# Optimization experiments

Measured on AMD Instinct MI355X. Metric: run time of the kernel, lower is better.

## Reference

```python
import jax, jax.numpy as jnp
import numpy as np

N, E, IN_DIM, HID, K, PDIM, NCLS, NHID_LAYERS = 50000, 800000, 128, 64, 3, 2, 16, 3
EPS = 1e-5


def setup_inputs() -> dict:
    key = jax.random.key(0)
    ks = jax.random.split(key, 24)
    d = {
        'feature': jax.random.normal(ks[0], (N, IN_DIM), jnp.float32),
        'emb_w': jax.random.normal(ks[1], (IN_DIM, HID), jnp.float32) * 0.05,
        'emb_b': jnp.zeros((HID,), jnp.float32),
        # 3 identical hidden GMM layers (stacked on leading axis)
        'fc_w': jax.random.normal(ks[2], (NHID_LAYERS, HID, K * HID), jnp.float32) * 0.05,
        'fc_b': jnp.zeros((NHID_LAYERS, K * HID), jnp.float32),
        'mu': jax.random.normal(ks[3], (NHID_LAYERS, K, PDIM), jnp.float32),
        'inv_sigma': jnp.ones((NHID_LAYERS, K, PDIM), jnp.float32) + 0.1 * jax.random.normal(ks[4], (NHID_LAYERS, K, PDIM), jnp.float32),
        'pp_w': jax.random.normal(ks[5], (NHID_LAYERS, 2, PDIM), jnp.float32),
        'pp_b': jnp.zeros((NHID_LAYERS, PDIM), jnp.float32),
        'bn_g': jnp.ones((NHID_LAYERS, HID), jnp.float32),
        'bn_b': jnp.zeros((NHID_LAYERS, HID), jnp.float32),
        # last layer: hidden -> n_classes
        'fc_w_l': jax.random.normal(ks[6], (HID, K * NCLS), jnp.float32) * 0.05,
        'fc_b_l': jnp.zeros((K * NCLS,), jnp.float32),
        'mu_l': jax.random.normal(ks[7], (K, PDIM), jnp.float32),
        'inv_sigma_l': jnp.ones((K, PDIM), jnp.float32) + 0.1 * jax.random.normal(ks[8], (K, PDIM), jnp.float32),
        'pp_w_l': jax.random.normal(ks[9], (2, PDIM), jnp.float32),
        'pp_b_l': jnp.zeros((PDIM,), jnp.float32),
        'bn_g_l': jnp.ones((NCLS,), jnp.float32),
        'bn_b_l': jnp.zeros((NCLS,), jnp.float32),
        'edge_index': jax.random.randint(ks[10], (2, E), 0, N, jnp.int64),
    }
    return d


def _gmm_layer(h, row, col, pseudo, fcw, fcb, mu, isg, bng, bnb, residual):
    n = h.shape[0]
    k, out = mu.shape[0], fcw.shape[1] // mu.shape[0]
    hp = (h @ fcw + fcb).reshape(n, k, out)          # [N,K,out]
    diff = pseudo[:, None, :] - mu                    # [E,K,2]
    gauss = jnp.exp(-0.5 * jnp.sum((diff * isg) ** 2, axis=-1))  # [E,K]
    msg = jnp.einsum('ek,ekc->ec', gauss, hp[row])    # gather src, weight, sum kernels
    agg = jax.ops.segment_sum(msg, col, num_segments=n)  # scatter-add to dst
    mean = jnp.mean(agg, axis=0)
    var = jnp.var(agg, axis=0)
    hbn = (agg - mean) * jax.lax.rsqrt(var + EPS) * bng + bnb  # BN (train stats)
    hnew = jax.nn.relu(hbn)
    if residual:
        hnew = h + hnew
    return hnew  # dropout p=0.0


def reference(feature, emb_w, emb_b, fc_w, fc_b, mu, inv_sigma, pp_w, pp_b, bn_g, bn_b,
              fc_w_l, fc_b_l, mu_l, inv_sigma_l, pp_w_l, pp_b_l, bn_g_l, bn_b_l, edge_index):
    row, col = edge_index[0], edge_index[1]
    n = feature.shape[0]
    ones_e = jnp.ones((row.shape[0],), feature.dtype)
    deg_r = jax.ops.segment_sum(ones_e, row, num_segments=n)
    deg_c = jax.ops.segment_sum(ones_e, col, num_segments=n)
    srcs = jax.lax.rsqrt(deg_r[row] + 1.0)
    dsts = jax.lax.rsqrt(deg_c[col] + 1.0)
    pseudo = jnp.stack([srcs, dsts], axis=-1)  # [E,2]
    h = feature @ emb_w + emb_b
    for i in range(NHID_LAYERS):
        ps = jnp.tanh(pseudo @ pp_w[i] + pp_b[i])
        h = _gmm_layer(h, row, col, ps, fc_w[i], fc_b[i], mu[i], inv_sigma[i], bn_g[i], bn_b[i], residual=True)
    ps = jnp.tanh(pseudo @ pp_w_l + pp_b_l)
    h = _gmm_layer(h, row, col, ps, fc_w_l, fc_b_l, mu_l, inv_sigma_l, bn_g_l, bn_b_l, residual=False)
    return h
```

## Files before the change

kernel.cpp:

```cpp
#include <hip/hip_runtime.h>
#include <cstdint>
#include <cstddef>


#define EPS 1e-5f
#define KAUG 196

__global__ void degree_kernel(const int* __restrict__ rowi, const int* __restrict__ coli,
                              int* __restrict__ dr, int* __restrict__ dc, int E) {
    int i = blockIdx.x * blockDim.x + threadIdx.x;
    int stride = gridDim.x * blockDim.x;
    for (; i < E; i += stride) {
        atomicAdd(&dr[rowi[i]], 1);
        atomicAdd(&dc[coli[i]], 1);
    }
}

__global__ void pseudo_kernel(const int* __restrict__ rowi, const int* __restrict__ coli,
                              const int* __restrict__ dr, const int* __restrict__ dc,
                              float2* __restrict__ pseudo, int E) {
    int i = blockIdx.x * blockDim.x + threadIdx.x;
    int stride = gridDim.x * blockDim.x;
    for (; i < E; i += stride) {
        float a = rsqrtf((float)dr[rowi[i]] + 1.0f);
        float b = rsqrtf((float)dc[coli[i]] + 1.0f);
        pseudo[i] = make_float2(a, b);
    }
}

__global__ __launch_bounds__(256) void scan_phase1(const int* __restrict__ cnt,
                                                   int* __restrict__ partial,
                                                   int* __restrict__ blockSum, int Nn) {
    __shared__ int sm[256];
    int tid = blockIdx.x * 256 + threadIdx.x;
    int v = (tid < Nn) ? cnt[tid] : 0;
    sm[threadIdx.x] = v;
    __syncthreads();
    for (int d = 1; d < 256; d <<= 1) {
        int t = (threadIdx.x >= d) ? sm[threadIdx.x - d] : 0;
        __syncthreads();
        sm[threadIdx.x] += t;
        __syncthreads();
    }
    if (tid < Nn) partial[tid] = sm[threadIdx.x] - v;
    if (threadIdx.x == 255) blockSum[blockIdx.x] = sm[255];
}

__global__ __launch_bounds__(1024) void scan_phase2(const int* __restrict__ blockSum,
                                                    int* __restrict__ blockOff, int B) {
    __shared__ int sm[1024];
    int v = (threadIdx.x < B) ? blockSum[threadIdx.x] : 0;
    sm[threadIdx.x] = v;
    __syncthreads();
    for (int d = 1; d < 1024; d <<= 1) {
        int t = (threadIdx.x >= d) ? sm[threadIdx.x - d] : 0;
        __syncthreads();
        sm[threadIdx.x] += t;
        __syncthreads();
    }
    if (threadIdx.x < B) blockOff[threadIdx.x] = sm[threadIdx.x] - v;
}

__global__ __launch_bounds__(256) void scan_phase3(const int* __restrict__ partial,
                                                   const int* __restrict__ blockOff,
                                                   int* __restrict__ start,
                                                   int* __restrict__ cursor, int Nn) {
    int tid = blockIdx.x * 256 + threadIdx.x;
    if (tid < Nn) {
        int s = partial[tid] + blockOff[blockIdx.x];
        start[tid] = s;
        cursor[tid] = s;
    }
}

__global__ void csr_scatter(const int* __restrict__ rowi, const int* __restrict__ coli,
                            const float2* __restrict__ pseudo, int* __restrict__ cursor,
                            int* __restrict__ rowPerm, float2* __restrict__ pseudoPerm, int E) {
    int i = blockIdx.x * blockDim.x + threadIdx.x;
    int stride = gridDim.x * blockDim.x;
    for (; i < E; i += stride) {
        int d = coli[i];
        int pos = atomicAdd(&cursor[d], 1);
        rowPerm[pos] = rowi[i];
        pseudoPerm[pos] = pseudo[i];
    }
}

__global__ void gauss_kernel(const float2* __restrict__ pseudo,
                             const float* __restrict__ ppw,
                             const float* __restrict__ ppb,
                             const float* __restrict__ mu,
                             const float* __restrict__ isg,
                             float4* __restrict__ gauss, int E) {
    int i = blockIdx.x * blockDim.x + threadIdx.x;
    int stride = gridDim.x * blockDim.x;
    float w00 = ppw[0], w01 = ppw[1], w10 = ppw[2], w11 = ppw[3];
    float b0 = ppb[0], b1 = ppb[1];
    float m00 = mu[0], m01 = mu[1], m10 = mu[2], m11 = mu[3], m20 = mu[4], m21 = mu[5];
    float s00 = isg[0], s01 = isg[1], s10 = isg[2], s11 = isg[3], s20 = isg[4], s21 = isg[5];
    for (; i < E; i += stride) {
        float2 p = pseudo[i];
        float ps0 = tanhf(fmaf(p.y, w10, fmaf(p.x, w00, b0)));
        float ps1 = tanhf(fmaf(p.y, w11, fmaf(p.x, w01, b1)));
        float d0, d1;
        d0 = (ps0 - m00) * s00; d1 = (ps1 - m01) * s01;
        float g0 = expf(-0.5f * (d0 * d0 + d1 * d1));
        d0 = (ps0 - m10) * s10; d1 = (ps1 - m11) * s11;
        float g1 = expf(-0.5f * (d0 * d0 + d1 * d1));
        d0 = (ps0 - m20) * s20; d1 = (ps1 - m21) * s21;
        float g2 = expf(-0.5f * (d0 * d0 + d1 * d1));
        gauss[i] = make_float4(g0, g1, g2, 0.0f);
    }
}

__global__ void w2_transform(const float* __restrict__ fcw, const float* __restrict__ fcb,
                             float* __restrict__ W2, int C) {
    int i = blockIdx.x * blockDim.x + threadIdx.x;
    int tot = KAUG * C;
    if (i >= tot) return;
    int r = i / C, c = i - r * C;
    float v;
    if (r < 192) {
        int k = r >> 6, j = r & 63;
        v = fcw[j * (3 * C) + k * C + c];
    } else if (r < 195) {
        v = fcb[(r - 192) * C + c];
    } else {
        v = 0.0f;
    }
    W2[i] = v;
}

__global__ __launch_bounds__(256) void pull_kernel(const int* __restrict__ start,
                                                   const int* __restrict__ cnt,
                                                   const int* __restrict__ rowPerm,
                                                   const float4* __restrict__ gauss,
                                                   const float* __restrict__ h,
                                                   float* __restrict__ m, int Nn) {
    int wave = threadIdx.x >> 6;
    int lane = threadIdx.x & 63;
    int d = blockIdx.x * 4 + wave;
    if (d >= Nn) return;
    int s = start[d];
    int e = s + cnt[d];
    float a0 = 0.0f, a1 = 0.0f, a2 = 0.0f;
    float s0 = 0.0f, s1 = 0.0f, s2 = 0.0f;
    const float* hl = h + lane;
    int i = s;
    for (; i + 3 < e; i += 4) {
        int r0 = rowPerm[i], r1 = rowPerm[i + 1], r2 = rowPerm[i + 2], r3 = rowPerm[i + 3];
        float4 g0 = gauss[i], g1 = gauss[i + 1], g2 = gauss[i + 2], g3 = gauss[i + 3];
        float h0 = hl[(size_t)r0 * 64], h1 = hl[(size_t)r1 * 64];
        float h2 = hl[(size_t)r2 * 64], h3 = hl[(size_t)r3 * 64];
        a0 = fmaf(g0.x, h0, a0); a1 = fmaf(g0.y, h0, a1); a2 = fmaf(g0.z, h0, a2);
        a0 = fmaf(g1.x, h1, a0); a1 = fmaf(g1.y, h1, a1); a2 = fmaf(g1.z, h1, a2);
        a0 = fmaf(g2.x, h2, a0); a1 = fmaf(g2.y, h2, a1); a2 = fmaf(g2.z, h2, a2);
        a0 = fmaf(g3.x, h3, a0); a1 = fmaf(g3.y, h3, a1); a2 = fmaf(g3.z, h3, a2);
        s0 += g0.x + g1.x + g2.x + g3.x;
        s1 += g0.y + g1.y + g2.y + g3.y;
        s2 += g0.z + g1.z + g2.z + g3.z;
    }
    for (; i < e; ++i) {
        int r0 = rowPerm[i];
        float4 g0 = gauss[i];
        float h0 = hl[(size_t)r0 * 64];
        a0 = fmaf(g0.x, h0, a0); a1 = fmaf(g0.y, h0, a1); a2 = fmaf(g0.z, h0, a2);
        s0 += g0.x; s1 += g0.y; s2 += g0.z;
    }
    float* mr = m + (size_t)d * KAUG;
    mr[lane] = a0;
    mr[64 + lane] = a1;
    mr[128 + lane] = a2;
    if (lane < 3) mr[192 + lane] = (lane == 0) ? s0 : ((lane == 1) ? s1 : s2);
    if (lane == 3) mr[195] = 0.0f;
}

template <int KDIM, int NC, int ROWS>
__global__ __launch_bounds__(256) void gemm_bias(const float* __restrict__ X,
                                                 const float* __restrict__ W,
                                                 const float* __restrict__ Bv,
                                                 float* __restrict__ Y, int M) {
    constexpr int TPR = 256 / ROWS;
    constexpr int CPT = NC / TPR;
    __shared__ __align__(16) float Ws[KDIM * NC];
    __shared__ float Bs[NC];
    __shared__ float Xs[ROWS][KDIM + 1];

    for (int i = threadIdx.x; i < KDIM * NC; i += 256) Ws[i] = W[i];
    if (Bv && threadIdx.x < NC) Bs[threadIdx.x] = Bv[threadIdx.x];
    int row0 = blockIdx.x * ROWS;
    for (int i = threadIdx.x; i < ROWS * KDIM; i += 256) {
        int r = i / KDIM, k = i - r * KDIM;
        int gr = row0 + r;
        Xs[r][k] = (gr < M) ? X[(size_t)gr * KDIM + k] : 0.0f;
    }
    __syncthreads();

    int r = threadIdx.x / TPR;
    int lc = threadIdx.x % TPR;
    int gr = row0 + r;
    if (gr >= M) return;

    float acc[CPT];
#pragma unroll
    for (int j = 0; j < CPT; ++j) acc[j] = Bv ? Bs[lc * CPT + j] : 0.0f;
    for (int k = 0; k < KDIM; ++k) {
        float xv = Xs[r][k];
        const float* wr = &Ws[k * NC + lc * CPT];
#pragma unroll
        for (int j = 0; j < CPT; ++j) acc[j] = fmaf(xv, wr[j], acc[j]);
    }
    float* yr = Y + (size_t)gr * NC + lc * CPT;
#pragma unroll
    for (int j = 0; j < CPT; ++j) yr[j] = acc[j];
}

template <int C>
__global__ __launch_bounds__(256) void bn_stats(const float* __restrict__ x, int Nn,
                                                float* __restrict__ sums) {
    constexpr int G = 256 / C;
    int c = threadIdx.x % C;
    int g = threadIdx.x / C;
    float s = 0.0f, ss = 0.0f;
    int totalG = gridDim.x * G;
    for (int r = blockIdx.x * G + g; r < Nn; r += totalG) {
        float v = x[(size_t)r * C + c];
        s += v;
        ss += v * v;
    }
    __shared__ float ls[256], lss[256];
    ls[threadIdx.x] = s;
    lss[threadIdx.x] = ss;
    __syncthreads();
    if (threadIdx.x < C) {
        float ts = 0.0f, tss = 0.0f;
#pragma unroll
        for (int gg = 0; gg < G; ++gg) {
            ts += ls[gg * C + threadIdx.x];
            tss += lss[gg * C + threadIdx.x];
        }
        atomicAdd(&sums[threadIdx.x], ts);
        atomicAdd(&sums[C + threadIdx.x], tss);
    }
}

template <int C, bool RES>
__global__ __launch_bounds__(256) void bn_apply(const float* __restrict__ agg,
                                                const float* __restrict__ sums,
                                                const float* __restrict__ gam,
                                                const float* __restrict__ bet,
                                                const float* __restrict__ hin,
                                                float* __restrict__ hout, int Nn) {
    size_t i = (size_t)blockIdx.x * blockDim.x + threadIdx.x;
    size_t tot = (size_t)Nn * C;
    size_t stride = (size_t)gridDim.x * blockDim.x;
    float invN = 1.0f / (float)Nn;
    for (; i < tot; i += stride) {
        int c = (int)(i & (C - 1));
        float mean = sums[c] * invN;
        float var = sums[C + c] * invN - mean * mean;
        float scale = gam[c] * rsqrtf(var + EPS);
        float v = (agg[i] - mean) * scale + bet[c];
        v = fmaxf(v, 0.0f);
        if (RES) v += hin[i];
        hout[i] = v;
    }
}

extern "C" void kernel_launch(void* const* d_in, const int* in_sizes, int n_in,
                              void* d_out, int out_size, void* d_ws, size_t ws_size,
                              hipStream_t stream) {
    const float* feature = (const float*)d_in[0];
    const float* emb_w = (const float*)d_in[1];
    const float* emb_b = (const float*)d_in[2];
    const float* fc_w = (const float*)d_in[3];
    const float* fc_b = (const float*)d_in[4];
    const float* mu = (const float*)d_in[5];
    const float* isg = (const float*)d_in[6];
    const float* pp_w = (const float*)d_in[7];
    const float* pp_b = (const float*)d_in[8];
    const float* bn_g = (const float*)d_in[9];
    const float* bn_b = (const float*)d_in[10];
    const float* fc_w_l = (const float*)d_in[11];
    const float* fc_b_l = (const float*)d_in[12];
    const float* mu_l = (const float*)d_in[13];
    const float* isg_l = (const float*)d_in[14];
    const float* pp_w_l = (const float*)d_in[15];
    const float* pp_b_l = (const float*)d_in[16];
    const float* bn_g_l = (const float*)d_in[17];
    const float* bn_b_l = (const float*)d_in[18];
    const int* edge = (const int*)d_in[19];

    const int N = in_sizes[0] / 128;
    const int E = in_sizes[19] / 2;
    const int* rowi = edge;
    const int* coli = edge + E;

    char* ws = (char*)d_ws;
    size_t off = 0;
    auto alloc = [&](size_t sz) -> void* {
        void* p = ws + off;
        off += (sz + 255) & ~(size_t)255;
        return p;
    };
    int* dr = (int*)alloc((size_t)N * 4);
    int* dc = (int*)alloc((size_t)N * 4);
    int* startv = (int*)alloc((size_t)N * 4);
    int* cursor = (int*)alloc((size_t)N * 4);
    int* partial = (int*)alloc((size_t)N * 4);
    int* blockSum = (int*)alloc(1024 * 4);
    int* blockOff = (int*)alloc(1024 * 4);
    float2* pseudo = (float2*)alloc((size_t)E * 8);
    float2* pseudoPerm = (float2*)alloc((size_t)E * 8);
    int* rowPerm = (int*)alloc((size_t)E * 4);
    float4* gauss = (float4*)alloc((size_t)E * 16);
    float* h = (float*)alloc((size_t)N * 64 * 4);
    float* m = (float*)alloc((size_t)N * KAUG * 4);
    float* agg = (float*)alloc((size_t)N * 64 * 4);
    float* W2 = (float*)alloc((size_t)KAUG * 64 * 4);
    float* sums = (float*)alloc(2 * 64 * 4);
    (void)ws_size;

    hipMemsetAsync(dr, 0, (size_t)N * 4, stream);
    hipMemsetAsync(dc, 0, (size_t)N * 4, stream);
    degree_kernel<<<2048, 256, 0, stream>>>(rowi, coli, dr, dc, E);
    pseudo_kernel<<<2048, 256, 0, stream>>>(rowi, coli, dr, dc, pseudo, E);

    const int scanB = (N + 255) / 256;
    scan_phase1<<<scanB, 256, 0, stream>>>(dc, partial, blockSum, N);
    scan_phase2<<<1, 1024, 0, stream>>>(blockSum, blockOff, scanB);
    scan_phase3<<<scanB, 256, 0, stream>>>(partial, blockOff, startv, cursor, N);

    csr_scatter<<<2048, 256, 0, stream>>>(rowi, coli, pseudo, cursor, rowPerm, pseudoPerm, E);

    gemm_bias<128, 64, 32><<<(N + 31) / 32, 256, 0, stream>>>(feature, emb_w, emb_b, h, N);

    const int pullBlocks = (N + 3) / 4;
    for (int i = 0; i < 3; ++i) {
        gauss_kernel<<<1024, 256, 0, stream>>>(pseudoPerm, pp_w + i * 4, pp_b + i * 2,
                                               mu + i * 6, isg + i * 6, gauss, E);
        w2_transform<<<(KAUG * 64 + 255) / 256, 256, 0, stream>>>(
            fc_w + (size_t)i * 64 * 192, fc_b + (size_t)i * 192, W2, 64);
        pull_kernel<<<pullBlocks, 256, 0, stream>>>(startv, dc, rowPerm, gauss, h, m, N);
        gemm_bias<KAUG, 64, 16><<<(N + 15) / 16, 256, 0, stream>>>(m, W2, nullptr, agg, N);
        hipMemsetAsync(sums, 0, 2 * 64 * 4, stream);
        bn_stats<64><<<256, 256, 0, stream>>>(agg, N, sums);
        bn_apply<64, true><<<2048, 256, 0, stream>>>(agg, sums, bn_g + i * 64, bn_b + i * 64,
                                                     h, h, N);
    }

    gauss_kernel<<<1024, 256, 0, stream>>>(pseudoPerm, pp_w_l, pp_b_l, mu_l, isg_l, gauss, E);
    w2_transform<<<(KAUG * 16 + 255) / 256, 256, 0, stream>>>(fc_w_l, fc_b_l, W2, 16);
    pull_kernel<<<pullBlocks, 256, 0, stream>>>(startv, dc, rowPerm, gauss, h, m, N);
    gemm_bias<KAUG, 16, 32><<<(N + 31) / 32, 256, 0, stream>>>(m, W2, nullptr, agg, N);
    hipMemsetAsync(sums, 0, 2 * 16 * 4, stream);
    bn_stats<16><<<256, 256, 0, stream>>>(agg, N, sums);
    bn_apply<16, false><<<2048, 256, 0, stream>>>(agg, sums, bn_g_l, bn_b_l, nullptr,
                                                  (float*)d_out, N);
}
```

Before: 785.7 us.

## Fuse gaussian weights into pull kernel and pack edge records

Removes the separate pseudo and per-layer gauss kernels. Pseudo-coordinates are now computed during the CSR scatter and stored with the source index in one packed float4 per edge. The pull kernel loads 64 edge records per wave, evaluates the gaussians in-lane, and shares them through LDS before the gather-accumulate. The sums memsets are folded into w2_transform. This saves E×16-byte gauss writes and reads per layer plus several launches, at the cost of redundant transcendental work being added to the latency-bound pull loop.

```diff
diff --git a/kernel.cpp b/kernel.cpp
--- a/kernel.cpp
+++ b/kernel.cpp
@@ -13,18 +13,6 @@
     for (; i < E; i += stride) {
         atomicAdd(&dr[rowi[i]], 1);
         atomicAdd(&dc[coli[i]], 1);
-    }
-}
-
-__global__ void pseudo_kernel(const int* __restrict__ rowi, const int* __restrict__ coli,
-                              const int* __restrict__ dr, const int* __restrict__ dc,
-                              float2* __restrict__ pseudo, int E) {
-    int i = blockIdx.x * blockDim.x + threadIdx.x;
-    int stride = gridDim.x * blockDim.x;
-    for (; i < E; i += stride) {
-        float a = rsqrtf((float)dr[rowi[i]] + 1.0f);
-        float b = rsqrtf((float)dc[coli[i]] + 1.0f);
-        pseudo[i] = make_float2(a, b);
     }
 }
 
@@ -74,48 +62,24 @@
 }
 
 __global__ void csr_scatter(const int* __restrict__ rowi, const int* __restrict__ coli,
-                            const float2* __restrict__ pseudo, int* __restrict__ cursor,
-                            int* __restrict__ rowPerm, float2* __restrict__ pseudoPerm, int E) {
+                            const int* __restrict__ dr, const int* __restrict__ dc,
+                            int* __restrict__ cursor, float4* __restrict__ perm, int E) {
     int i = blockIdx.x * blockDim.x + threadIdx.x;
     int stride = gridDim.x * blockDim.x;
     for (; i < E; i += stride) {
+        int r = rowi[i];
         int d = coli[i];
         int pos = atomicAdd(&cursor[d], 1);
-        rowPerm[pos] = rowi[i];
-        pseudoPerm[pos] = pseudo[i];
-    }
-}
-
-__global__ void gauss_kernel(const float2* __restrict__ pseudo,
-                             const float* __restrict__ ppw,
-                             const float* __restrict__ ppb,
-                             const float* __restrict__ mu,
-                             const float* __restrict__ isg,
-                             float4* __restrict__ gauss, int E) {
+        float a = rsqrtf((float)dr[r] + 1.0f);
+        float b = rsqrtf((float)dc[d] + 1.0f);
+        perm[pos] = make_float4(__int_as_float(r), a, b, 0.0f);
+    }
+}
+
+__global__ void w2_transform(const float* __restrict__ fcw, const float* __restrict__ fcb,
+                             float* __restrict__ W2, float* __restrict__ sums, int C) {
     int i = blockIdx.x * blockDim.x + threadIdx.x;
-    int stride = gridDim.x * blockDim.x;
-    float w00 = ppw[0], w01 = ppw[1], w10 = ppw[2], w11 = ppw[3];
-    float b0 = ppb[0], b1 = ppb[1];
-    float m00 = mu[0], m01 = mu[1], m10 = mu[2], m11 = mu[3], m20 = mu[4], m21 = mu[5];
-    float s00 = isg[0], s01 = isg[1], s10 = isg[2], s11 = isg[3], s20 = isg[4], s21 = isg[5];
-    for (; i < E; i += stride) {
-        float2 p = pseudo[i];
-        float ps0 = tanhf(fmaf(p.y, w10, fmaf(p.x, w00, b0)));
-        float ps1 = tanhf(fmaf(p.y, w11, fmaf(p.x, w01, b1)));
-        float d0, d1;
-        d0 = (ps0 - m00) * s00; d1 = (ps1 - m01) * s01;
-        float g0 = expf(-0.5f * (d0 * d0 + d1 * d1));
-        d0 = (ps0 - m10) * s10; d1 = (ps1 - m11) * s11;
-        float g1 = expf(-0.5f * (d0 * d0 + d1 * d1));
-        d0 = (ps0 - m20) * s20; d1 = (ps1 - m21) * s21;
-        float g2 = expf(-0.5f * (d0 * d0 + d1 * d1));
-        gauss[i] = make_float4(g0, g1, g2, 0.0f);
-    }
-}
-
-__global__ void w2_transform(const float* __restrict__ fcw, const float* __restrict__ fcb,
-                             float* __restrict__ W2, int C) {
-    int i = blockIdx.x * blockDim.x + threadIdx.x;
+    if (i < 128) sums[i] = 0.0f;
     int tot = KAUG * C;
     if (i >= tot) return;
     int r = i / C, c = i - r * C;
@@ -133,45 +97,74 @@
 
 __global__ __launch_bounds__(256) void pull_kernel(const int* __restrict__ start,
                                                    const int* __restrict__ cnt,
-                                                   const int* __restrict__ rowPerm,
-                                                   const float4* __restrict__ gauss,
+                                                   const float4* __restrict__ perm,
+                                                   const float* __restrict__ ppw,
+                                                   const float* __restrict__ ppb,
+                                                   const float* __restrict__ mu,
+                                                   const float* __restrict__ isg,
                                                    const float* __restrict__ h,
                                                    float* __restrict__ m, int Nn) {
-    int wave = threadIdx.x >> 6;
+    __shared__ float4 gl[4][64];
+    int wv = threadIdx.x >> 6;
     int lane = threadIdx.x & 63;
-    int d = blockIdx.x * 4 + wave;
+    int d = blockIdx.x * 4 + wv;
     if (d >= Nn) return;
+    float w00 = ppw[0], w01 = ppw[1], w10 = ppw[2], w11 = ppw[3];
+    float b0 = ppb[0], b1 = ppb[1];
+    float m00 = mu[0], m01 = mu[1], m10 = mu[2], m11 = mu[3], m20 = mu[4], m21 = mu[5];
+    float s00 = isg[0], s01 = isg[1], s10 = isg[2], s11 = isg[3], s20 = isg[4], s21 = isg[5];
+
     int s = start[d];
     int e = s + cnt[d];
     float a0 = 0.0f, a1 = 0.0f, a2 = 0.0f;
-    float s0 = 0.0f, s1 = 0.0f, s2 = 0.0f;
+    float g0s = 0.0f, g1s = 0.0f, g2s = 0.0f;
     const float* hl = h + lane;
-    int i = s;
-    for (; i + 3 < e; i += 4) {
-        int r0 = rowPerm[i], r1 = rowPerm[i + 1], r2 = rowPerm[i + 2], r3 = rowPerm[i + 3];
-        float4 g0 = gauss[i], g1 = gauss[i + 1], g2 = gauss[i + 2], g3 = gauss[i + 3];
-        float h0 = hl[(size_t)r0 * 64], h1 = hl[(size_t)r1 * 64];
-        float h2 = hl[(size_t)r2 * 64], h3 = hl[(size_t)r3 * 64];
-        a0 = fmaf(g0.x, h0, a0); a1 = fmaf(g0.y, h0, a1); a2 = fmaf(g0.z, h0, a2);
-        a0 = fmaf(g1.x, h1, a0); a1 = fmaf(g1.y, h1, a1); a2 = fmaf(g1.z, h1, a2);
-        a0 = fmaf(g2.x, h2, a0); a1 = fmaf(g2.y, h2, a1); a2 = fmaf(g2.z, h2, a2);
-        a0 = fmaf(g3.x, h3, a0); a1 = fmaf(g3.y, h3, a1); a2 = fmaf(g3.z, h3, a2);
-        s0 += g0.x + g1.x + g2.x + g3.x;
-        s1 += g0.y + g1.y + g2.y + g3.y;
-        s2 += g0.z + g1.z + g2.z + g3.z;
-    }
-    for (; i < e; ++i) {
-        int r0 = rowPerm[i];
-        float4 g0 = gauss[i];
-        float h0 = hl[(size_t)r0 * 64];
-        a0 = fmaf(g0.x, h0, a0); a1 = fmaf(g0.y, h0, a1); a2 = fmaf(g0.z, h0, a2);
-        s0 += g0.x; s1 += g0.y; s2 += g0.z;
+
+    for (int base = s; base < e; base += 64) {
+        int idx = base + lane;
+        float4 rec = make_float4(0.0f, 0.0f, 0.0f, 0.0f);
+        if (idx < e) rec = perm[idx];
+        float ps0 = tanhf(fmaf(rec.z, w10, fmaf(rec.y, w00, b0)));
+        float ps1 = tanhf(fmaf(rec.z, w11, fmaf(rec.y, w01, b1)));
+        float d0, d1;
+        d0 = (ps0 - m00) * s00; d1 = (ps1 - m01) * s01;
+        float g0 = expf(-0.5f * (d0 * d0 + d1 * d1));
+        d0 = (ps0 - m10) * s10; d1 = (ps1 - m11) * s11;
+        float g1 = expf(-0.5f * (d0 * d0 + d1 * d1));
+        d0 = (ps0 - m20) * s20; d1 = (ps1 - m21) * s21;
+        float g2 = expf(-0.5f * (d0 * d0 + d1 * d1));
+        gl[wv][lane] = make_float4(g0, g1, g2, rec.x);
+
+        int cb = e - base;
+        if (cb > 64) cb = 64;
+        int j = 0;
+        for (; j + 3 < cb; j += 4) {
+            float4 q0 = gl[wv][j], q1 = gl[wv][j + 1], q2 = gl[wv][j + 2], q3 = gl[wv][j + 3];
+            int r0 = __float_as_int(q0.w), r1 = __float_as_int(q1.w);
+            int r2 = __float_as_int(q2.w), r3 = __float_as_int(q3.w);
+            float h0 = hl[(size_t)r0 * 64], h1 = hl[(size_t)r1 * 64];
+            float h2 = hl[(size_t)r2 * 64], h3 = hl[(size_t)r3 * 64];
+            a0 = fmaf(q0.x, h0, a0); a1 = fmaf(q0.y, h0, a1); a2 = fmaf(q0.z, h0, a2);
+            a0 = fmaf(q1.x, h1, a0); a1 = fmaf(q1.y, h1, a1); a2 = fmaf(q1.z, h1, a2);
+            a0 = fmaf(q2.x, h2, a0); a1 = fmaf(q2.y, h2, a1); a2 = fmaf(q2.z, h2, a2);
+            a0 = fmaf(q3.x, h3, a0); a1 = fmaf(q3.y, h3, a1); a2 = fmaf(q3.z, h3, a2);
+            g0s += q0.x + q1.x + q2.x + q3.x;
+            g1s += q0.y + q1.y + q2.y + q3.y;
+            g2s += q0.z + q1.z + q2.z + q3.z;
+        }
+        for (; j < cb; ++j) {
+            float4 q0 = gl[wv][j];
+            int r0 = __float_as_int(q0.w);
+            float h0 = hl[(size_t)r0 * 64];
+            a0 = fmaf(q0.x, h0, a0); a1 = fmaf(q0.y, h0, a1); a2 = fmaf(q0.z, h0, a2);
+            g0s += q0.x; g1s += q0.y; g2s += q0.z;
+        }
     }
     float* mr = m + (size_t)d * KAUG;
     mr[lane] = a0;
     mr[64 + lane] = a1;
     mr[128 + lane] = a2;
-    if (lane < 3) mr[192 + lane] = (lane == 0) ? s0 : ((lane == 1) ? s1 : s2);
+    if (lane < 3) mr[192 + lane] = (lane == 0) ? g0s : ((lane == 1) ? g1s : g2s);
     if (lane == 3) mr[195] = 0.0f;
 }
 
@@ -310,10 +303,7 @@
     int* partial = (int*)alloc((size_t)N * 4);
     int* blockSum = (int*)alloc(1024 * 4);
     int* blockOff = (int*)alloc(1024 * 4);
-    float2* pseudo = (float2*)alloc((size_t)E * 8);
-    float2* pseudoPerm = (float2*)alloc((size_t)E * 8);
-    int* rowPerm = (int*)alloc((size_t)E * 4);
-    float4* gauss = (float4*)alloc((size_t)E * 16);
+    float4* perm = (float4*)alloc((size_t)E * 16);
     float* h = (float*)alloc((size_t)N * 64 * 4);
     float* m = (float*)alloc((size_t)N * KAUG * 4);
     float* agg = (float*)alloc((size_t)N * 64 * 4);
@@ -324,36 +314,33 @@
     hipMemsetAsync(dr, 0, (size_t)N * 4, stream);
     hipMemsetAsync(dc, 0, (size_t)N * 4, stream);
     degree_kernel<<<2048, 256, 0, stream>>>(rowi, coli, dr, dc, E);
-    pseudo_kernel<<<2048, 256, 0, stream>>>(rowi, coli, dr, dc, pseudo, E);
 
     const int scanB = (N + 255) / 256;
     scan_phase1<<<scanB, 256, 0, stream>>>(dc, partial, blockSum, N);
     scan_phase2<<<1, 1024, 0, stream>>>(blockSum, blockOff, scanB);
     scan_phase3<<<scanB, 256, 0, stream>>>(partial, blockOff, startv, cursor, N);
 
-    csr_scatter<<<2048, 256, 0, stream>>>(rowi, coli, pseudo, cursor, rowPerm, pseudoPerm, E);
+    csr_scatter<<<2048, 256, 0, stream>>>(rowi, coli, dr, dc, cursor, perm, E);
 
     gemm_bias<128, 64, 32><<<(N + 31) / 32, 256, 0, stream>>>(feature, emb_w, emb_b, h, N);
 
     const int pullBlocks = (N + 3) / 4;
     for (int i = 0; i < 3; ++i) {
-        gauss_kernel<<<1024, 256, 0, stream>>>(pseudoPerm, pp_w + i * 4, pp_b + i * 2,
-                                               mu + i * 6, isg + i * 6, gauss, E);
         w2_transform<<<(KAUG * 64 + 255) / 256, 256, 0, stream>>>(
-            fc_w + (size_t)i * 64 * 192, fc_b + (size_t)i * 192, W2, 64);
-        pull_kernel<<<pullBlocks, 256, 0, stream>>>(startv, dc, rowPerm, gauss, h, m, N);
+            fc_w + (size_t)i * 64 * 192, fc_b + (size_t)i * 192, W2, sums, 64);
+        pull_kernel<<<pullBlocks, 256, 0, stream>>>(startv, dc, perm,
+                                                    pp_w + i * 4, pp_b + i * 2,
+                                                    mu + i * 6, isg + i * 6, h, m, N);
         gemm_bias<KAUG, 64, 16><<<(N + 15) / 16, 256, 0, stream>>>(m, W2, nullptr, agg, N);
-        hipMemsetAsync(sums, 0, 2 * 64 * 4, stream);
         bn_stats<64><<<256, 256, 0, stream>>>(agg, N, sums);
         bn_apply<64, true><<<2048, 256, 0, stream>>>(agg, sums, bn_g + i * 64, bn_b + i * 64,
                                                      h, h, N);
     }
 
-    gauss_kernel<<<1024, 256, 0, stream>>>(pseudoPerm, pp_w_l, pp_b_l, mu_l, isg_l, gauss, E);
-    w2_transform<<<(KAUG * 16 + 255) / 256, 256, 0, stream>>>(fc_w_l, fc_b_l, W2, 16);
-    pull_kernel<<<pullBlocks, 256, 0, stream>>>(startv, dc, rowPerm, gauss, h, m, N);
+    w2_transform<<<(KAUG * 16 + 255) / 256, 256, 0, stream>>>(fc_w_l, fc_b_l, W2, sums, 16);
+    pull_kernel<<<pullBlocks, 256, 0, stream>>>(startv, dc, perm,
+                                                pp_w_l, pp_b_l, mu_l, isg_l, h, m, N);
     gemm_bias<KAUG, 16, 32><<<(N + 31) / 32, 256, 0, stream>>>(m, W2, nullptr, agg, N);
-    hipMemsetAsync(sums, 0, 2 * 16 * 4, stream);
     bn_stats<16><<<256, 256, 0, stream>>>(agg, N, sums);
     bn_apply<16, false><<<2048, 256, 0, stream>>>(agg, sums, bn_g_l, bn_b_l, nullptr,
                                                   (float*)d_out, N);
```

New measurement: 703.5 us. 1.12x faster.
